# Kernel optimization log

Hardware: AMD Instinct MI355X
Metric: run time of the kernel (lower is better)

## Reference

```python
import jax, jax.numpy as jnp
import numpy as np

# Module hyperparameters (match init_kwargs)
T0, Z0, T1, Z1, K, S, ROUTING = 4, 16, 8, 16, 5, 1, 3
PAD = 2  # hard-coded padding=2 in the torch module
N, H, W_SP = 4, 128, 128


def setup_inputs() -> dict:
    key = jax.random.key(0)
    k1, k2 = jax.random.split(key)
    u = jax.random.normal(k1, (N, T0, Z0, H, W_SP), dtype=jnp.float32)
    # t_0 independent Conv2d(z_0 -> t_1*z_1, k, s, padding=2, bias=False) weights
    W = jax.random.normal(k2, (T0, T1 * Z1, Z0, K, K), dtype=jnp.float32) * 0.05
    return {"u": u, "W": W}


def _squash(p):
    # squash along last (z_1) axis, matching torch: p_norm = sqrt(|p|^2 + 1e-9)
    n2 = jnp.sum(p * p, axis=-1, keepdims=True)
    n = jnp.sqrt(n2 + 1e-9)
    return n2 / (1.0 + n2) * p / n


def _capsule_convs(u, W):
    # t_0 independent convs == one grouped conv with feature_group_count=t_0
    n, t0, z0, h, w = u.shape
    x = u.reshape(n, t0 * z0, h, w)
    wk = W.reshape(t0 * T1 * Z1, z0, K, K)
    y = jax.lax.conv_general_dilated(
        x, wk, window_strides=(S, S), padding=[(PAD, PAD), (PAD, PAD)],
        dimension_numbers=("NCHW", "OIHW", "NCHW"), feature_group_count=t0)
    h1, w1 = y.shape[2], y.shape[3]
    # [N, t0*t1*z1, H1, W1] -> u_hat [t0, N, H1, W1, t1, z1]
    y = y.reshape(n, t0, T1, Z1, h1, w1)
    return jnp.transpose(y, (1, 0, 4, 5, 2, 3))


def _routing(u_hat):
    t0, n, h, w, t1, z1 = u_hat.shape
    dt = u_hat.dtype
    b = jnp.zeros((t0, n, t1, h, w), dt)  # NCHW layout per capsule type
    neg_inf = jnp.array(-jnp.inf, dt)
    zero = jnp.array(0.0, dt)
    win = (1, 1, 1, K, K)
    ones = (1, 1, 1, 1, 1)
    pad = [(0, 0), (0, 0), (0, 0), (PAD, PAD), (PAD, PAD)]
    v = None
    for d in range(ROUTING):
        uh = jax.lax.stop_gradient(u_hat) if d < ROUTING - 1 else u_hat
        # stability max: max_pool2d(k,1,pad=2) (pads with -inf) then max over t1
        b_max = jax.lax.reduce_window(b, neg_inf, jax.lax.max, win, ones, pad)
        b_max = jnp.max(b_max, axis=2, keepdims=True)
        c = jnp.exp(b - b_max)  # [t0, N, t1, H, W]
        # conv2d_same with ones kernel [1,t1,k,k] == channel-sum then kxk box-sum
        sum_c = jax.lax.reduce_window(jnp.sum(c, axis=2, keepdims=True), zero,
                                      jax.lax.add, win, ones, pad)
        r = c / sum_c                                   # [t0, N, t1, H, W]
        r = jnp.transpose(r, (0, 1, 3, 4, 2))[..., None]  # [t0,N,H,W,t1,1]
        p = jnp.sum(r * uh, axis=0)                     # [N, H, W, t1, z1]
        v = _squash(p)
        # NOTE: the original torch code computes b + (u_hat*v).sum(4) into a
        # list `b_t_list_` that is never assigned back, so b stays zero across
        # iterations. We faithfully reproduce that (no b update).
    return jnp.transpose(v, (0, 3, 4, 1, 2))  # [N, t1, z1, H, W]


def reference(u, W):
    return _routing(_capsule_convs(u, W))
```

## Files before the change

### kernel.cpp

```cpp
#include <hip/hip_runtime.h>
#include <hip/hip_bf16.h>


#define CO 128

typedef __attribute__((ext_vector_type(8))) short bf16x8;
typedef __attribute__((ext_vector_type(4))) float f32x4;

__global__ __launch_bounds__(256) void k_reorder(const float* __restrict__ Wsrc,
                                                 ushort* __restrict__ Wr2) {
    int idx = blockIdx.x * 256 + threadIdx.x;
    if (idx >= 25 * 128 * 64) return;
    int ci = idx & 63;
    int r  = idx >> 6;
    int co = r & 127;
    int kk = r >> 7;
    int t0 = ci >> 4, z0 = ci & 15;
    __hip_bfloat16 b = __float2bfloat16(Wsrc[((t0 * CO + co) * 16 + z0) * 25 + kk]);
    Wr2[idx] = *(ushort*)&b;
}

__global__ __launch_bounds__(256) void k_pre(const float* __restrict__ u,
                                             ushort* __restrict__ ut) {
    __shared__ float lt[64][65];
    int b = blockIdx.x;
    int wc = b & 1; int nh = b >> 1; int h = nh & 127; int n = nh >> 7;
    int w0 = wc * 64;
    int t = threadIdx.x;
    int w = t & 63; int cg = t >> 6;
    const float* up = u + (size_t)n * (64 * 128 * 128) + h * 128 + w0 + w;
#pragma unroll
    for (int i = 0; i < 16; ++i) {
        int ci = cg * 16 + i;
        lt[w][ci] = up[(size_t)ci * (128 * 128)];
    }
    __syncthreads();
    int ci2 = t & 63; int pg = t >> 6;
    ushort* op = ut + (((size_t)(n * 128 + h)) * 128 + w0) * 64 + ci2;
#pragma unroll
    for (int i = 0; i < 16; ++i) {
        int w2 = pg * 16 + i;
        __hip_bfloat16 bv = __float2bfloat16(lt[w2][ci2]);
        op[(size_t)w2 * 64] = *(ushort*)&bv;
    }
}

__global__ __launch_bounds__(256) void k_caps(const ushort* __restrict__ ut,
                                              const ushort* __restrict__ Wr2,
                                              float* __restrict__ out) {
    __shared__ ushort As[240 * 80];
    __shared__ ushort Bs[128 * 80];

    int tid = threadIdx.x;
    int bid = blockIdx.x;
    int bx = bid & 7, by = (bid >> 3) & 15, n = bid >> 7;
    int h0 = by * 8, w0 = bx * 16;

    for (int i = tid; i < 1920; i += 256) {
        int p = i >> 3, c = i & 7;
        int rr = p / 20, cc = p - rr * 20;
        int hh = h0 + rr - 2, ww = w0 + cc - 2;
        bf16x8 v = {};
        if ((unsigned)hh < 128u && (unsigned)ww < 128u)
            v = *(const bf16x8*)(ut + (((size_t)(n * 128 + hh)) * 128 + ww) * 64 + c * 8);
        *(bf16x8*)&As[p * 80 + c * 8] = v;
    }

    int lane = tid & 63, wid = tid >> 6;
    int wm4  = (wid >> 1) * 4;
    int wn64 = (wid & 1) * 64;
    int q = lane >> 4, m16 = lane & 15;

    f32x4 acc[4][4] = {};

    bf16x8 pre[4];
#pragma unroll
    for (int j = 0; j < 4; ++j)
        pre[j] = *(const bf16x8*)(Wr2 + (size_t)(tid + j * 256) * 8);

    int aBase = (wm4 * 20 + m16) * 80 + q * 8;
    int bBase = (wn64 + m16) * 80 + q * 8;

#pragma unroll
    for (int kk = 0; kk < 25; ++kk) {
        const int kh = kk / 5, kw = kk % 5;
        __syncthreads();
#pragma unroll
        for (int j = 0; j < 4; ++j) {
            int i = tid + j * 256;
            *(bf16x8*)&Bs[(i >> 3) * 80 + (i & 7) * 8] = pre[j];
        }
        __syncthreads();
        if (kk < 24) {
#pragma unroll
            for (int j = 0; j < 4; ++j)
                pre[j] = *(const bf16x8*)(Wr2 + (size_t)(kk + 1) * 8192 + (tid + j * 256) * 8);
        }
#pragma unroll
        for (int ks = 0; ks < 2; ++ks) {
            bf16x8 a[4], bb[4];
#pragma unroll
            for (int mi = 0; mi < 4; ++mi)
                a[mi] = *(const bf16x8*)&As[aBase + ((mi + kh) * 20 + kw) * 80 + ks * 32];
#pragma unroll
            for (int ni = 0; ni < 4; ++ni)
                bb[ni] = *(const bf16x8*)&Bs[bBase + ni * (16 * 80) + ks * 32];
#pragma unroll
            for (int mi = 0; mi < 4; ++mi)
#pragma unroll
                for (int ni = 0; ni < 4; ++ni)
                    acc[mi][ni] = __builtin_amdgcn_mfma_f32_16x16x32_bf16(
                        a[mi], bb[ni], acc[mi][ni], 0, 0, 0);
        }
    }

#pragma unroll
    for (int mi = 0; mi < 4; ++mi) {
        int h = h0 + wm4 + mi;
        int hlo = h - 2; if (hlo < 0) hlo = 0;
        int hhi = h + 2; if (hhi > 127) hhi = 127;
        float cnth = (float)(hhi - hlo + 1);
#pragma unroll
        for (int ni = 0; ni < 4; ++ni) {
            f32x4 cv = acc[mi][ni];
            float ov[4];
#pragma unroll
            for (int reg = 0; reg < 4; ++reg) {
                int w = w0 + q * 4 + reg;
                int wlo = w - 2; if (wlo < 0) wlo = 0;
                int whi = w + 2; if (whi > 127) whi = 127;
                float s = 1.f / (8.f * cnth * (float)(whi - wlo + 1));
                float pv = cv[reg] * s;
                float n2 = pv * pv;
                n2 += __shfl_xor(n2, 1);
                n2 += __shfl_xor(n2, 2);
                n2 += __shfl_xor(n2, 4);
                n2 += __shfl_xor(n2, 8);
                float fac = n2 / ((1.f + n2) * sqrtf(n2 + 1e-9f));
                ov[reg] = pv * fac;
            }
            int co = wn64 + ni * 16 + m16;
            *(float4*)(out + (((size_t)(n * CO + co)) << 14) + h * 128 + w0 + q * 4) =
                make_float4(ov[0], ov[1], ov[2], ov[3]);
        }
    }
}

extern "C" void kernel_launch(void* const* d_in, const int* in_sizes, int n_in,
                              void* d_out, int out_size, void* d_ws, size_t ws_size,
                              hipStream_t stream) {
    const float* u    = (const float*)d_in[0];
    const float* Wsrc = (const float*)d_in[1];
    float* out = (float*)d_out;
    ushort* Wr2 = (ushort*)d_ws;
    ushort* ut  = (ushort*)((char*)d_ws + 409600);

    k_reorder<<<800, 256, 0, stream>>>(Wsrc, Wr2);
    k_pre<<<1024, 256, 0, stream>>>(u, ut);
    k_caps<<<512, 256, 0, stream>>>(ut, Wr2, out);
}
```

Measured before the change: 108.3 us.

## Merge prep kernels, vectorize transpose, load conv weights directly into registers

The weight reorder and input transpose kernels become one launch whose blocks split by index, which removes one kernel launch. The transpose now reads float4 and writes 16-byte bf16 vectors. In the main conv kernel the B weight tile no longer goes through shared memory: each wave loads its MFMA B fragments straight from global memory into registers, prefetching the next tap one step ahead. This drops two barriers per tap, in exchange for higher register pressure and redundant global loads across waves.

```diff
diff --git a/kernel.cpp b/kernel.cpp
--- a/kernel.cpp
+++ b/kernel.cpp
@@ -7,41 +7,52 @@
 typedef __attribute__((ext_vector_type(8))) short bf16x8;
 typedef __attribute__((ext_vector_type(4))) float f32x4;
 
-__global__ __launch_bounds__(256) void k_reorder(const float* __restrict__ Wsrc,
-                                                 ushort* __restrict__ Wr2) {
-    int idx = blockIdx.x * 256 + threadIdx.x;
-    if (idx >= 25 * 128 * 64) return;
-    int ci = idx & 63;
-    int r  = idx >> 6;
-    int co = r & 127;
-    int kk = r >> 7;
-    int t0 = ci >> 4, z0 = ci & 15;
-    __hip_bfloat16 b = __float2bfloat16(Wsrc[((t0 * CO + co) * 16 + z0) * 25 + kk]);
-    Wr2[idx] = *(ushort*)&b;
-}
-
-__global__ __launch_bounds__(256) void k_pre(const float* __restrict__ u,
-                                             ushort* __restrict__ ut) {
+__global__ __launch_bounds__(256) void k_prep(const float* __restrict__ u,
+                                              const float* __restrict__ Wsrc,
+                                              ushort* __restrict__ ut,
+                                              ushort* __restrict__ Wr2) {
     __shared__ float lt[64][65];
     int b = blockIdx.x;
+    int t = threadIdx.x;
+    if (b < 800) {
+        int idx = b * 256 + t;
+        int ci = idx & 63;
+        int r  = idx >> 6;
+        int co = r & 127;
+        int kk = r >> 7;
+        int t0 = ci >> 4, z0 = ci & 15;
+        __hip_bfloat16 bb = __float2bfloat16(Wsrc[((t0 * CO + co) * 16 + z0) * 25 + kk]);
+        Wr2[idx] = *(ushort*)&bb;
+        return;
+    }
+    b -= 800;
     int wc = b & 1; int nh = b >> 1; int h = nh & 127; int n = nh >> 7;
     int w0 = wc * 64;
-    int t = threadIdx.x;
-    int w = t & 63; int cg = t >> 6;
-    const float* up = u + (size_t)n * (64 * 128 * 128) + h * 128 + w0 + w;
+    int ciL = t >> 4;
+    int wl  = (t & 15) * 4;
+    const float* up = u + (size_t)n * (64 * 128 * 128) + h * 128 + w0;
 #pragma unroll
-    for (int i = 0; i < 16; ++i) {
-        int ci = cg * 16 + i;
-        lt[w][ci] = up[(size_t)ci * (128 * 128)];
+    for (int p = 0; p < 4; ++p) {
+        int ci = p * 16 + ciL;
+        float4 v = *(const float4*)(up + (size_t)ci * 16384 + wl);
+        lt[wl + 0][ci] = v.x;
+        lt[wl + 1][ci] = v.y;
+        lt[wl + 2][ci] = v.z;
+        lt[wl + 3][ci] = v.w;
     }
     __syncthreads();
-    int ci2 = t & 63; int pg = t >> 6;
-    ushort* op = ut + (((size_t)(n * 128 + h)) * 128 + w0) * 64 + ci2;
+    ushort* op = ut + (((size_t)(n * 128 + h)) * 128 + w0) * 64;
 #pragma unroll
-    for (int i = 0; i < 16; ++i) {
-        int w2 = pg * 16 + i;
-        __hip_bfloat16 bv = __float2bfloat16(lt[w2][ci2]);
-        op[(size_t)w2 * 64] = *(ushort*)&bv;
+    for (int p = 0; p < 2; ++p) {
+        int item = p * 256 + t;
+        int c8 = item & 7, w2 = item >> 3;
+        bf16x8 vv;
+#pragma unroll
+        for (int j = 0; j < 8; ++j) {
+            __hip_bfloat16 bb = __float2bfloat16(lt[w2][c8 * 8 + j]);
+            vv[j] = *(ushort*)&bb;
+        }
+        *(bf16x8*)(op + (size_t)w2 * 64 + c8 * 8) = vv;
     }
 }
 
@@ -49,12 +60,25 @@
                                               const ushort* __restrict__ Wr2,
                                               float* __restrict__ out) {
     __shared__ ushort As[240 * 80];
-    __shared__ ushort Bs[128 * 80];
 
     int tid = threadIdx.x;
     int bid = blockIdx.x;
     int bx = bid & 7, by = (bid >> 3) & 15, n = bid >> 7;
     int h0 = by * 8, w0 = bx * 16;
+
+    int lane = tid & 63, wid = tid >> 6;
+    int wm4  = (wid >> 1) * 4;
+    int wn64 = (wid & 1) * 64;
+    int q = lane >> 4, m16 = lane & 15;
+
+    const ushort* bp = Wr2 + (size_t)(wn64 + m16) * 64 + q * 8;
+
+    bf16x8 bc[2][4];
+#pragma unroll
+    for (int ks = 0; ks < 2; ++ks)
+#pragma unroll
+        for (int ni = 0; ni < 4; ++ni)
+            bc[ks][ni] = *(const bf16x8*)(bp + ni * 1024 + ks * 32);
 
     for (int i = tid; i < 1920; i += 256) {
         int p = i >> 3, c = i & 7;
@@ -65,52 +89,45 @@
             v = *(const bf16x8*)(ut + (((size_t)(n * 128 + hh)) * 128 + ww) * 64 + c * 8);
         *(bf16x8*)&As[p * 80 + c * 8] = v;
     }
+    __syncthreads();
 
-    int lane = tid & 63, wid = tid >> 6;
-    int wm4  = (wid >> 1) * 4;
-    int wn64 = (wid & 1) * 64;
-    int q = lane >> 4, m16 = lane & 15;
+    int aBase = (wm4 * 20 + m16) * 80 + q * 8;
 
     f32x4 acc[4][4] = {};
 
-    bf16x8 pre[4];
+    for (int kh = 0; kh < 5; ++kh) {
 #pragma unroll
-    for (int j = 0; j < 4; ++j)
-        pre[j] = *(const bf16x8*)(Wr2 + (size_t)(tid + j * 256) * 8);
-
-    int aBase = (wm4 * 20 + m16) * 80 + q * 8;
-    int bBase = (wn64 + m16) * 80 + q * 8;
-
+        for (int kw = 0; kw < 5; ++kw) {
+            bf16x8 bn[2][4];
+            bool pf = (kw < 4) || (kh < 4);
+            if (pf) {
+                const ushort* np = bp + (size_t)(kh * 5 + kw + 1) * 8192;
 #pragma unroll
-    for (int kk = 0; kk < 25; ++kk) {
-        const int kh = kk / 5, kw = kk % 5;
-        __syncthreads();
+                for (int ks = 0; ks < 2; ++ks)
 #pragma unroll
-        for (int j = 0; j < 4; ++j) {
-            int i = tid + j * 256;
-            *(bf16x8*)&Bs[(i >> 3) * 80 + (i & 7) * 8] = pre[j];
-        }
-        __syncthreads();
-        if (kk < 24) {
+                    for (int ni = 0; ni < 4; ++ni)
+                        bn[ks][ni] = *(const bf16x8*)(np + ni * 1024 + ks * 32);
+            }
 #pragma unroll
-            for (int j = 0; j < 4; ++j)
-                pre[j] = *(const bf16x8*)(Wr2 + (size_t)(kk + 1) * 8192 + (tid + j * 256) * 8);
-        }
+            for (int ks = 0; ks < 2; ++ks) {
+                bf16x8 a[4];
 #pragma unroll
-        for (int ks = 0; ks < 2; ++ks) {
-            bf16x8 a[4], bb[4];
+                for (int mi = 0; mi < 4; ++mi)
+                    a[mi] = *(const bf16x8*)&As[aBase + ((mi + kh) * 20 + kw) * 80 + ks * 32];
 #pragma unroll
-            for (int mi = 0; mi < 4; ++mi)
-                a[mi] = *(const bf16x8*)&As[aBase + ((mi + kh) * 20 + kw) * 80 + ks * 32];
+                for (int mi = 0; mi < 4; ++mi)
 #pragma unroll
-            for (int ni = 0; ni < 4; ++ni)
-                bb[ni] = *(const bf16x8*)&Bs[bBase + ni * (16 * 80) + ks * 32];
+                    for (int ni = 0; ni < 4; ++ni)
+                        acc[mi][ni] = __builtin_amdgcn_mfma_f32_16x16x32_bf16(
+                            a[mi], bc[ks][ni], acc[mi][ni], 0, 0, 0);
+            }
+            if (pf) {
 #pragma unroll
-            for (int mi = 0; mi < 4; ++mi)
+                for (int ks = 0; ks < 2; ++ks)
 #pragma unroll
-                for (int ni = 0; ni < 4; ++ni)
-                    acc[mi][ni] = __builtin_amdgcn_mfma_f32_16x16x32_bf16(
-                        a[mi], bb[ni], acc[mi][ni], 0, 0, 0);
+                    for (int ni = 0; ni < 4; ++ni)
+                        bc[ks][ni] = bn[ks][ni];
+            }
         }
     }
 
@@ -155,7 +172,6 @@
     ushort* Wr2 = (ushort*)d_ws;
     ushort* ut  = (ushort*)((char*)d_ws + 409600);
 
-    k_reorder<<<800, 256, 0, stream>>>(Wsrc, Wr2);
-    k_pre<<<1024, 256, 0, stream>>>(u, ut);
+    k_prep<<<1824, 256, 0, stream>>>(u, Wsrc, ut, Wr2);
     k_caps<<<512, 256, 0, stream>>>(ut, Wr2, out);
 }
```

Measured after the change: 140.6 us. +29.8%, slower.

## Fuse input transpose into conv kernel and stream MFMA-ordered weights into registers

Applied to the files above, without the earlier changes.

Removes the separate NHWC bf16 pre-transpose kernel, so the conv kernel now reads fp32 NCHW input directly, converts it to bf16 and fills the shared-memory halo tile. Weights are pre-reordered into the per-lane MFMA fragment layout and loaded straight from global memory into double-buffered registers. This drops the shared-memory B tile and the two barriers per kernel tap. The cost is strided, uncoalesced global reads during the halo fill (8 channel-strided scalar loads per thread), plus more register pressure from holding 16 bf16x8 weight fragments. The A tile row stride also shrinks from 80 to 68.

```diff
diff --git a/kernel.cpp b/kernel.cpp
--- a/kernel.cpp
+++ b/kernel.cpp
@@ -8,111 +8,95 @@
 typedef __attribute__((ext_vector_type(4))) float f32x4;
 
 __global__ __launch_bounds__(256) void k_reorder(const float* __restrict__ Wsrc,
-                                                 ushort* __restrict__ Wr2) {
+                                                 ushort* __restrict__ Wr2b) {
     int idx = blockIdx.x * 256 + threadIdx.x;
-    if (idx >= 25 * 128 * 64) return;
     int ci = idx & 63;
     int r  = idx >> 6;
     int co = r & 127;
     int kk = r >> 7;
     int t0 = ci >> 4, z0 = ci & 15;
-    __hip_bfloat16 b = __float2bfloat16(Wsrc[((t0 * CO + co) * 16 + z0) * 25 + kk]);
-    Wr2[idx] = *(ushort*)&b;
+    __hip_bfloat16 bb = __float2bfloat16(Wsrc[((t0 * CO + co) * 16 + z0) * 25 + kk]);
+    int cg = co >> 6, ni = (co >> 4) & 3, m16 = co & 15;
+    int ks = ci >> 5, q = (ci >> 3) & 3, j = ci & 7;
+    int oi = ((((kk * 2 + cg) * 2 + ks) * 4 + ni) << 9) + ((q * 16 + m16) << 3) + j;
+    Wr2b[oi] = *(ushort*)&bb;
 }
 
-__global__ __launch_bounds__(256) void k_pre(const float* __restrict__ u,
-                                             ushort* __restrict__ ut) {
-    __shared__ float lt[64][65];
-    int b = blockIdx.x;
-    int wc = b & 1; int nh = b >> 1; int h = nh & 127; int n = nh >> 7;
-    int w0 = wc * 64;
-    int t = threadIdx.x;
-    int w = t & 63; int cg = t >> 6;
-    const float* up = u + (size_t)n * (64 * 128 * 128) + h * 128 + w0 + w;
-#pragma unroll
-    for (int i = 0; i < 16; ++i) {
-        int ci = cg * 16 + i;
-        lt[w][ci] = up[(size_t)ci * (128 * 128)];
-    }
-    __syncthreads();
-    int ci2 = t & 63; int pg = t >> 6;
-    ushort* op = ut + (((size_t)(n * 128 + h)) * 128 + w0) * 64 + ci2;
-#pragma unroll
-    for (int i = 0; i < 16; ++i) {
-        int w2 = pg * 16 + i;
-        __hip_bfloat16 bv = __float2bfloat16(lt[w2][ci2]);
-        op[(size_t)w2 * 64] = *(ushort*)&bv;
-    }
-}
-
-__global__ __launch_bounds__(256) void k_caps(const ushort* __restrict__ ut,
-                                              const ushort* __restrict__ Wr2,
+__global__ __launch_bounds__(256) void k_caps(const float* __restrict__ u,
+                                              const ushort* __restrict__ Wr2b,
                                               float* __restrict__ out) {
-    __shared__ ushort As[240 * 80];
-    __shared__ ushort Bs[128 * 80];
+    __shared__ ushort As[240 * 68];
 
     int tid = threadIdx.x;
     int bid = blockIdx.x;
     int bx = bid & 7, by = (bid >> 3) & 15, n = bid >> 7;
     int h0 = by * 8, w0 = bx * 16;
 
+    int lane = tid & 63, wid = tid >> 6;
+    int rg = wid >> 1;
+    int cg = wid & 1;
+    int wm4  = rg * 4;
+    int wn64 = cg * 64;
+    int q = lane >> 4, m16 = lane & 15;
+
+    const ushort* wp = Wr2b + ((size_t)cg * 4096) + lane * 8;
+
+    bf16x8 bA[8], bB[8];
+#define LOADB(dst, kk2)                                                  \
+    {                                                                    \
+        _Pragma("unroll") for (int ks_ = 0; ks_ < 2; ++ks_)              \
+            _Pragma("unroll") for (int ni_ = 0; ni_ < 4; ++ni_)          \
+                dst[ks_ * 4 + ni_] = *(const bf16x8*)(                   \
+                    wp + (size_t)(kk2) * 8192 + (ks_ * 4 + ni_) * 512);  \
+    }
+
+    LOADB(bA, 0);
+
     for (int i = tid; i < 1920; i += 256) {
         int p = i >> 3, c = i & 7;
         int rr = p / 20, cc = p - rr * 20;
         int hh = h0 + rr - 2, ww = w0 + cc - 2;
         bf16x8 v = {};
-        if ((unsigned)hh < 128u && (unsigned)ww < 128u)
-            v = *(const bf16x8*)(ut + (((size_t)(n * 128 + hh)) * 128 + ww) * 64 + c * 8);
-        *(bf16x8*)&As[p * 80 + c * 8] = v;
+        if (((unsigned)hh < 128u) & ((unsigned)ww < 128u)) {
+            const float* up = u + (size_t)n * (64 * 128 * 128) + (size_t)hh * 128 + ww;
+#pragma unroll
+            for (int j = 0; j < 8; ++j) {
+                __hip_bfloat16 bb = __float2bfloat16(up[(size_t)(c * 8 + j) * 16384]);
+                v[j] = *(ushort*)&bb;
+            }
+        }
+        *(bf16x8*)&As[p * 68 + c * 8] = v;
     }
+    __syncthreads();
+    LOADB(bB, 1);
 
-    int lane = tid & 63, wid = tid >> 6;
-    int wm4  = (wid >> 1) * 4;
-    int wn64 = (wid & 1) * 64;
-    int q = lane >> 4, m16 = lane & 15;
+    const ushort* ap = As + (wm4 * 20 + m16) * 68 + q * 8;
 
     f32x4 acc[4][4] = {};
-
-    bf16x8 pre[4];
-#pragma unroll
-    for (int j = 0; j < 4; ++j)
-        pre[j] = *(const bf16x8*)(Wr2 + (size_t)(tid + j * 256) * 8);
-
-    int aBase = (wm4 * 20 + m16) * 80 + q * 8;
-    int bBase = (wn64 + m16) * 80 + q * 8;
 
 #pragma unroll
     for (int kk = 0; kk < 25; ++kk) {
         const int kh = kk / 5, kw = kk % 5;
-        __syncthreads();
-#pragma unroll
-        for (int j = 0; j < 4; ++j) {
-            int i = tid + j * 256;
-            *(bf16x8*)&Bs[(i >> 3) * 80 + (i & 7) * 8] = pre[j];
-        }
-        __syncthreads();
-        if (kk < 24) {
-#pragma unroll
-            for (int j = 0; j < 4; ++j)
-                pre[j] = *(const bf16x8*)(Wr2 + (size_t)(kk + 1) * 8192 + (tid + j * 256) * 8);
-        }
 #pragma unroll
         for (int ks = 0; ks < 2; ++ks) {
-            bf16x8 a[4], bb[4];
+            bf16x8 a[4];
 #pragma unroll
             for (int mi = 0; mi < 4; ++mi)
-                a[mi] = *(const bf16x8*)&As[aBase + ((mi + kh) * 20 + kw) * 80 + ks * 32];
-#pragma unroll
-            for (int ni = 0; ni < 4; ++ni)
-                bb[ni] = *(const bf16x8*)&Bs[bBase + ni * (16 * 80) + ks * 32];
+                a[mi] = *(const bf16x8*)(ap + ((mi + kh) * 20 + kw) * 68 + ks * 32);
 #pragma unroll
             for (int mi = 0; mi < 4; ++mi)
 #pragma unroll
                 for (int ni = 0; ni < 4; ++ni)
                     acc[mi][ni] = __builtin_amdgcn_mfma_f32_16x16x32_bf16(
-                        a[mi], bb[ni], acc[mi][ni], 0, 0, 0);
+                        a[mi], (kk & 1) ? bB[ks * 4 + ni] : bA[ks * 4 + ni],
+                        acc[mi][ni], 0, 0, 0);
+        }
+        if (kk < 23) {
+            if (kk & 1) { LOADB(bB, kk + 2); }
+            else        { LOADB(bA, kk + 2); }
         }
     }
+#undef LOADB
 
 #pragma unroll
     for (int mi = 0; mi < 4; ++mi) {
@@ -152,10 +136,8 @@
     const float* u    = (const float*)d_in[0];
     const float* Wsrc = (const float*)d_in[1];
     float* out = (float*)d_out;
-    ushort* Wr2 = (ushort*)d_ws;
-    ushort* ut  = (ushort*)((char*)d_ws + 409600);
+    ushort* Wr2b = (ushort*)d_ws;
 
-    k_reorder<<<800, 256, 0, stream>>>(Wsrc, Wr2);
-    k_pre<<<1024, 256, 0, stream>>>(u, ut);
-    k_caps<<<512, 256, 0, stream>>>(ut, Wr2, out);
+    k_reorder<<<800, 256, 0, stream>>>(Wsrc, Wr2b);
+    k_caps<<<512, 256, 0, stream>>>(u, Wr2b, out);
 }
```

After: 117.1 us. 8.1% more time.
